# Kernel tuning notes

Hardware: AMD Instinct MI355X
Metric: run time of the kernel (lower is better)

## Reference

```python
import jax, jax.numpy as jnp
import numpy as np

D_IN = 768
D_OUT = 768
N_HEADS = 12
HEAD_DIM = D_OUT // N_HEADS


def setup_inputs() -> dict:
    key = jax.random.key(0)
    ks = jax.random.split(key, 6)
    B, S = 2, 4096
    x = jax.random.normal(ks[0], (B, S, D_IN), dtype=jnp.float32)
    s = 0.02
    Wq = jax.random.normal(ks[1], (D_IN, D_OUT), dtype=jnp.float32) * s
    Wk = jax.random.normal(ks[2], (D_IN, D_OUT), dtype=jnp.float32) * s
    Wv = jax.random.normal(ks[3], (D_IN, D_OUT), dtype=jnp.float32) * s
    Wo = jax.random.normal(ks[4], (D_OUT, D_OUT), dtype=jnp.float32) * s
    bo = jnp.zeros((D_OUT,), dtype=jnp.float32)
    return {"x": x, "Wq": Wq, "Wk": Wk, "Wv": Wv, "Wo": Wo, "bo": bo}


def reference(x, Wq, Wk, Wv, Wo, bo):
    B, S, _ = x.shape
    # QKV projections (no bias), reshape to [B, H, S, Dh]
    q = (x @ Wq).reshape(B, S, N_HEADS, HEAD_DIM).transpose(0, 2, 1, 3)
    k = (x @ Wk).reshape(B, S, N_HEADS, HEAD_DIM).transpose(0, 2, 1, 3)
    v = (x @ Wv).reshape(B, S, N_HEADS, HEAD_DIM).transpose(0, 2, 1, 3)
    # scores: [B, H, S, S], causal mask, scaled softmax
    scores = jnp.einsum('bhqd,bhkd->bhqk', q, k)
    causal = jnp.triu(jnp.ones((S, S), dtype=bool), k=1)
    scores = jnp.where(causal, -jnp.inf, scores)
    attn = jax.nn.softmax(scores / np.sqrt(HEAD_DIM).astype(np.float32), axis=-1)
    # dropout p=0.0 -> identity
    ctx = jnp.einsum('bhqk,bhkd->bqhd', attn, v).reshape(B, S, D_OUT)
    return ctx @ Wo + bo
```

## Files before the change

kernel.cpp:

```cpp
#include <hip/hip_runtime.h>

#define S 4096
#define BATCH 2
#define D 768
#define NH 12
#define DH 64
#define NROWS (BATCH * S)
#define N_ITEMS (32 * NH * BATCH)
#define CTR_OFF 67633152

typedef __attribute__((ext_vector_type(8))) short bf16x8;
typedef __attribute__((ext_vector_type(4))) float f32x4;
typedef __attribute__((ext_vector_type(2))) unsigned uint32x2;

__device__ __forceinline__ unsigned short f2bf(float f) {
    unsigned u = __builtin_bit_cast(unsigned, f);
    u += 0x7fff + ((u >> 16) & 1);
    return (unsigned short)(u >> 16);
}

__device__ __forceinline__ float fexp2(float x) {
#if __has_builtin(__builtin_amdgcn_exp2f)
    return __builtin_amdgcn_exp2f(x);
#else
    return exp2f(x);
#endif
}

#define GLDS16(g, l)                                                   \
    __builtin_amdgcn_global_load_lds(                                  \
        (const __attribute__((address_space(1))) void*)(g),            \
        (__attribute__((address_space(3))) void*)(l), 16, 0, 0)

__global__ __launch_bounds__(256) void cvt_x(const float* __restrict__ x,
                                             unsigned short* __restrict__ xb)
{
    int i = (blockIdx.x * 256 + threadIdx.x) * 4;
    float4 v = *(const float4*)(x + i);
    ushort4 o = make_ushort4(f2bf(v.x), f2bf(v.y), f2bf(v.z), f2bf(v.w));
    *(ushort4*)(xb + i) = o;
}

__global__ __launch_bounds__(256) void cvt_w(
    const float* __restrict__ Wq, const float* __restrict__ Wk,
    const float* __restrict__ Wv, const float* __restrict__ Wo,
    unsigned short* __restrict__ wt)
{
    __shared__ float tile[32][33];
    const int z = blockIdx.z;
    const float* W = (z == 0) ? Wq : (z == 1) ? Wk : (z == 2) ? Wv : Wo;
    const int k0 = blockIdx.x * 32, n0 = blockIdx.y * 32;
    const int t = threadIdx.x;
    const int r = t >> 3, c4 = (t & 7) * 4;

    float4 v = *(const float4*)(W + (size_t)(k0 + r) * D + n0 + c4);
    tile[r][c4 + 0] = v.x; tile[r][c4 + 1] = v.y;
    tile[r][c4 + 2] = v.z; tile[r][c4 + 3] = v.w;
    __syncthreads();
    ushort4 o = make_ushort4(f2bf(tile[c4 + 0][r]), f2bf(tile[c4 + 1][r]),
                             f2bf(tile[c4 + 2][r]), f2bf(tile[c4 + 3][r]));
    *(ushort4*)(wt + ((size_t)z * D + n0 + r) * D + k0 + c4) = o;
}

__global__ __launch_bounds__(256) void gemm_qkv(
    const unsigned short* __restrict__ xb,
    const unsigned short* __restrict__ wt,
    unsigned short* __restrict__ qb, unsigned short* __restrict__ kb,
    unsigned short* __restrict__ vtb)
{
    __shared__ unsigned short As[128 * 64];
    __shared__ unsigned short Bs[128 * 64];

    const int t = threadIdx.x;
    const int lane = t & 63, w = t >> 6;
    const int l16 = lane & 15, quad = lane >> 4;
    const int wm = w & 1, wn = w >> 1;
    const int m0 = blockIdx.x * 128;
    const int n0g = blockIdx.y * 128;
    const int z = n0g / 768;
    const int c0 = n0g - z * 768;
    const unsigned short* Wz = wt + (size_t)z * D * D;

    f32x4 acc[4][4] = {};

    for (int k0 = 0; k0 < D; k0 += 64) {
#pragma unroll
        for (int i = 0; i < 4; ++i) {
            int g = i * 256 + w * 64 + lane;
            int row = g >> 3, cl = g & 7, cg = cl ^ (row & 7);
            GLDS16(xb + (size_t)(m0 + row) * D + k0 + cg * 8,
                   As + (size_t)(i * 256 + w * 64) * 8);
            GLDS16(Wz + (size_t)(c0 + row) * D + k0 + cg * 8,
                   Bs + (size_t)(i * 256 + w * 64) * 8);
        }
        __syncthreads();
#pragma unroll
        for (int kk = 0; kk < 2; ++kk) {
            bf16x8 af[4], bf_[4];
#pragma unroll
            for (int mt = 0; mt < 4; ++mt) {
                int r = wm * 64 + mt * 16 + l16;
                int c = kk * 4 + quad;
                af[mt] = *(const bf16x8*)&As[(r * 8 + (c ^ (r & 7))) * 8];
            }
#pragma unroll
            for (int nt = 0; nt < 4; ++nt) {
                int r = wn * 64 + nt * 16 + l16;
                int c = kk * 4 + quad;
                bf_[nt] = *(const bf16x8*)&Bs[(r * 8 + (c ^ (r & 7))) * 8];
            }
#pragma unroll
            for (int mt = 0; mt < 4; ++mt)
#pragma unroll
                for (int nt = 0; nt < 4; ++nt)
                    acc[mt][nt] = __builtin_amdgcn_mfma_f32_16x16x32_bf16(
                        af[mt], bf_[nt], acc[mt][nt], 0, 0, 0);
        }
        __syncthreads();
    }

    if (z < 2) {
        unsigned short* outp = (z == 0) ? qb : kb;
        const float scale = (z == 0) ? 0.18033688011112042f : 1.0f;
#pragma unroll
        for (int mt = 0; mt < 4; ++mt) {
#pragma unroll
            for (int reg = 0; reg < 4; ++reg) {
                int m = wm * 64 + mt * 16 + quad * 4 + reg;
                int ng = m0 + m;
                int b = ng >> 12, s = ng & 4095;
#pragma unroll
                for (int nt = 0; nt < 4; ++nt) {
                    int n = c0 + wn * 64 + nt * 16 + l16;
                    int h = n >> 6, dh = n & 63;
                    outp[(((size_t)b * NH + h) * S + s) * DH + dh] =
                        f2bf(acc[mt][nt][reg] * scale);
                }
            }
        }
    } else {
#pragma unroll
        for (int mt = 0; mt < 4; ++mt) {
#pragma unroll
            for (int nt = 0; nt < 4; ++nt) {
                int m = wm * 64 + mt * 16 + quad * 4;
                int ng = m0 + m;
                int b = ng >> 12, s = ng & 4095;
                int n = c0 + wn * 64 + nt * 16 + l16;
                int h = n >> 6, dh = n & 63;
                ushort4 p = make_ushort4(
                    f2bf(acc[mt][nt][0]), f2bf(acc[mt][nt][1]),
                    f2bf(acc[mt][nt][2]), f2bf(acc[mt][nt][3]));
                *(ushort4*)(vtb + (((size_t)b * NH + h) * DH + dh) * S + s) = p;
            }
        }
    }
}

__global__ __launch_bounds__(512, 4) void attn_mfma(
    const unsigned short* __restrict__ qg,
    const unsigned short* __restrict__ kg,
    const unsigned short* __restrict__ vtg,
    unsigned short* __restrict__ ctxb,
    int* __restrict__ work_ctr)
{
    __shared__ unsigned short Ks[2][64 * 64];
    __shared__ unsigned short Vs[2][64 * 64];
    __shared__ int s_item;

    const float INF = __builtin_inff();
    const int t = threadIdx.x;
    const int w = t >> 6, lane = t & 63;
    const int l16 = lane & 15, quad = lane >> 4;
    const int a7 = l16 & 7;
    const int srow = t >> 3;
    const int scg = (t & 7) ^ (srow & 7);

    bf16x8 vone;
#pragma unroll
    for (int i = 0; i < 8; ++i) vone[i] = (short)0x3F80;

    for (;;) {
        if (t == 0) s_item = atomicAdd(work_ctr, 1);
        __syncthreads();
        const int p = s_item;
        if (p >= N_ITEMS) return;

        const int qt = 31 - (p / (NH * BATCH));
        const int hb = p % (NH * BATCH);
        const int h = hb % NH, b = hb / NH;
        const size_t hbase = ((size_t)b * NH + h) * (size_t)S * DH;
        const unsigned short* kp = kg + hbase;
        const unsigned short* vp = vtg + hbase;

        const int qrow = qt * 128 + w * 16 + l16;
        bf16x8 bq[2];
#pragma unroll
        for (int kk = 0; kk < 2; ++kk)
            bq[kk] = *(const bf16x8*)(qg + hbase + (size_t)qrow * DH +
                                      kk * 32 + quad * 8);

        f32x4 acc_o[4] = {};
        f32x4 acc_sum = {};

        const int jmax = 2 * qt + 1, jd = 2 * qt;

        GLDS16(kp + (size_t)srow * DH + scg * 8, &Ks[0][(size_t)w * 64 * 8]);
        GLDS16(vp + (size_t)srow * S + scg * 8, &Vs[0][(size_t)w * 64 * 8]);

        for (int j = 0; j <= jmax; ++j) {
            const int cur = j & 1;
            __syncthreads();
            if (j < jmax) {
                GLDS16(kp + (size_t)((j + 1) * 64 + srow) * DH + scg * 8,
                       &Ks[cur ^ 1][(size_t)w * 64 * 8]);
                GLDS16(vp + (size_t)srow * S + (j + 1) * 64 + scg * 8,
                       &Vs[cur ^ 1][(size_t)w * 64 * 8]);
            }

            const unsigned short* Kc = Ks[cur];
            const unsigned short* Vc = Vs[cur];

            f32x4 acc_s[4] = {};
            __builtin_amdgcn_s_setprio(1);
#pragma unroll
            for (int kk = 0; kk < 2; ++kk)
#pragma unroll
                for (int ms = 0; ms < 4; ++ms) {
                    int r = ms * 16 + l16, c = kk * 4 + quad;
                    bf16x8 ak = *(const bf16x8*)&Kc[(r * 8 + (c ^ a7)) * 8];
                    acc_s[ms] = __builtin_amdgcn_mfma_f32_16x16x32_bf16(
                        ak, bq[kk], acc_s[ms], 0, 0, 0);
                }
            __builtin_amdgcn_s_setprio(0);

            if (j >= jd) {
#pragma unroll
                for (int ms = 0; ms < 4; ++ms)
#pragma unroll
                    for (int reg = 0; reg < 4; ++reg)
                        if ((j * 64 + ms * 16 + quad * 4 + reg) > qrow)
                            acc_s[ms][reg] = -INF;
            }

            bf16x8 bp[2];
            {
                unsigned ulo[4], uhi[4];
#pragma unroll
                for (int ms = 0; ms < 4; ++ms) {
                    float e0 = fexp2(acc_s[ms][0]);
                    float e1 = fexp2(acc_s[ms][1]);
                    float e2 = fexp2(acc_s[ms][2]);
                    float e3 = fexp2(acc_s[ms][3]);
                    asm("v_cvt_pk_bf16_f32 %0, %1, %2"
                        : "=v"(ulo[ms]) : "v"(e0), "v"(e1));
                    asm("v_cvt_pk_bf16_f32 %0, %1, %2"
                        : "=v"(uhi[ms]) : "v"(e2), "v"(e3));
                }
#pragma unroll
                for (int kp2 = 0; kp2 < 2; ++kp2) {
                    uint32x2 lo = __builtin_amdgcn_permlane32_swap(
                        ulo[2 * kp2], ulo[2 * kp2 + 1], false, false);
                    uint32x2 s02 = __builtin_amdgcn_permlane16_swap(
                        lo[0], lo[1], false, false);
                    uint32x2 hi = __builtin_amdgcn_permlane32_swap(
                        uhi[2 * kp2], uhi[2 * kp2 + 1], false, false);
                    uint32x2 s13 = __builtin_amdgcn_permlane16_swap(
                        hi[0], hi[1], false, false);
                    union { unsigned u[4]; bf16x8 v; } pb;
                    pb.u[0] = s02[0]; pb.u[1] = s13[0];
                    pb.u[2] = s02[1]; pb.u[3] = s13[1];
                    bp[kp2] = pb.v;
                }
            }

            __builtin_amdgcn_s_setprio(1);
#pragma unroll
            for (int kk = 0; kk < 2; ++kk) {
#pragma unroll
                for (int d = 0; d < 4; ++d) {
                    int r = d * 16 + l16, c = kk * 4 + quad;
                    bf16x8 av = *(const bf16x8*)&Vc[(r * 8 + (c ^ a7)) * 8];
                    acc_o[d] = __builtin_amdgcn_mfma_f32_16x16x32_bf16(
                        av, bp[kk], acc_o[d], 0, 0, 0);
                }
                acc_sum = __builtin_amdgcn_mfma_f32_16x16x32_bf16(
                    vone, bp[kk], acc_sum, 0, 0, 0);
            }
            __builtin_amdgcn_s_setprio(0);
        }

        {
            float inv = 1.f / acc_sum[0];
            size_t base = ((size_t)(b * S + qrow)) * D + h * 64;
#pragma unroll
            for (int d = 0; d < 4; ++d) {
                ushort4 o;
                o.x = f2bf(acc_o[d][0] * inv);
                o.y = f2bf(acc_o[d][1] * inv);
                o.z = f2bf(acc_o[d][2] * inv);
                o.w = f2bf(acc_o[d][3] * inv);
                *(ushort4*)(ctxb + base + d * 16 + quad * 4) = o;
            }
        }
    }
}

__global__ __launch_bounds__(256) void gemm_out(
    const unsigned short* __restrict__ ctxb,
    const unsigned short* __restrict__ wt,
    const float* __restrict__ bo,
    float* __restrict__ out)
{
    __shared__ unsigned short As[128 * 64];
    __shared__ unsigned short Bs[64 * 64];

    const int t = threadIdx.x;
    const int lane = t & 63, w = t >> 6;
    const int l16 = lane & 15, quad = lane >> 4;
    const int m0 = blockIdx.x * 128;
    const int n0 = blockIdx.y * 64;
    const unsigned short* Wz = wt + (size_t)3 * D * D;

    f32x4 acc[2][4] = {};

    for (int k0 = 0; k0 < D; k0 += 64) {
#pragma unroll
        for (int i = 0; i < 4; ++i) {
            int g = i * 256 + w * 64 + lane;
            int row = g >> 3, cl = g & 7, cg = cl ^ (row & 7);
            GLDS16(ctxb + (size_t)(m0 + row) * D + k0 + cg * 8,
                   As + (size_t)(i * 256 + w * 64) * 8);
            if (i < 2)
                GLDS16(Wz + (size_t)(n0 + row) * D + k0 + cg * 8,
                       Bs + (size_t)(i * 256 + w * 64) * 8);
        }
        __syncthreads();
#pragma unroll
        for (int kk = 0; kk < 2; ++kk) {
            bf16x8 af[2], bf_[4];
#pragma unroll
            for (int mt = 0; mt < 2; ++mt) {
                int r = w * 32 + mt * 16 + l16;
                int c = kk * 4 + quad;
                af[mt] = *(const bf16x8*)&As[(r * 8 + (c ^ (r & 7))) * 8];
            }
#pragma unroll
            for (int nt = 0; nt < 4; ++nt) {
                int r = nt * 16 + l16;
                int c = kk * 4 + quad;
                bf_[nt] = *(const bf16x8*)&Bs[(r * 8 + (c ^ (r & 7))) * 8];
            }
#pragma unroll
            for (int mt = 0; mt < 2; ++mt)
#pragma unroll
                for (int nt = 0; nt < 4; ++nt)
                    acc[mt][nt] = __builtin_amdgcn_mfma_f32_16x16x32_bf16(
                        af[mt], bf_[nt], acc[mt][nt], 0, 0, 0);
        }
        __syncthreads();
    }

    float bv[4];
#pragma unroll
    for (int nt = 0; nt < 4; ++nt)
        bv[nt] = bo[n0 + nt * 16 + l16];
#pragma unroll
    for (int mt = 0; mt < 2; ++mt)
#pragma unroll
        for (int reg = 0; reg < 4; ++reg) {
            int m = m0 + w * 32 + mt * 16 + quad * 4 + reg;
#pragma unroll
            for (int nt = 0; nt < 4; ++nt)
                out[(size_t)m * D + n0 + nt * 16 + l16] =
                    acc[mt][nt][reg] + bv[nt];
        }
}

extern "C" void kernel_launch(void* const* d_in, const int* in_sizes, int n_in,
                              void* d_out, int out_size, void* d_ws, size_t ws_size,
                              hipStream_t stream)
{
    const float* x  = (const float*)d_in[0];
    const float* Wq = (const float*)d_in[1];
    const float* Wk = (const float*)d_in[2];
    const float* Wv = (const float*)d_in[3];
    const float* Wo = (const float*)d_in[4];
    const float* bo = (const float*)d_in[5];
    float* out = (float*)d_out;

    const size_t elems = (size_t)NROWS * D;
    unsigned short* xb   = (unsigned short*)d_ws;
    unsigned short* wt   = xb + elems;
    unsigned short* q    = wt + (size_t)4 * D * D;
    unsigned short* k    = q + elems;
    unsigned short* vt   = k + elems;
    unsigned short* ctxb = vt + elems;
    int* work_ctr = (int*)((char*)d_ws + CTR_OFF);

    hipMemsetAsync(work_ctr, 0, sizeof(int), stream);

    cvt_x<<<NROWS * D / 1024, 256, 0, stream>>>(x, xb);
    dim3 gw(D / 32, D / 32, 4);
    cvt_w<<<gw, 256, 0, stream>>>(Wq, Wk, Wv, Wo, wt);

    dim3 g1(NROWS / 128, (3 * D) / 128);
    gemm_qkv<<<g1, 256, 0, stream>>>(xb, wt, q, k, vt);

    attn_mfma<<<512, 512, 0, stream>>>(q, k, vt, ctxb, work_ctr);

    dim3 g3(NROWS / 128, D / 64);
    gemm_out<<<g3, 256, 0, stream>>>(ctxb, wt, bo, out);
}
```

Baseline: 232.9 us.

## Split KV range for longest causal query tiles and merge halves in combine kernel

The dynamic work queue now has 960 items instead of 768. The eight longest query tiles per head and batch are split into two halves of the KV range, and the remaining tiles are scheduled in decreasing length order. Each split half writes unnormalized fp32 output and row sums into scratch space reused from the x and weight conversion buffers. A new combine kernel adds the two halves and normalizes them into ctxb. The aim is to shorten the tail caused by long causal tiles. The cost is an extra kernel launch and roughly 12 MB of extra fp32 partial traffic.

```diff
diff --git a/kernel.cpp b/kernel.cpp
--- a/kernel.cpp
+++ b/kernel.cpp
@@ -6,8 +6,10 @@
 #define NH 12
 #define DH 64
 #define NROWS (BATCH * S)
-#define N_ITEMS (32 * NH * BATCH)
 #define CTR_OFF 67633152
+
+#define N_ITEMS 960
+#define NSPLIT 192
 
 typedef __attribute__((ext_vector_type(8))) short bf16x8;
 typedef __attribute__((ext_vector_type(4))) float f32x4;
@@ -162,6 +164,8 @@
     const unsigned short* __restrict__ kg,
     const unsigned short* __restrict__ vtg,
     unsigned short* __restrict__ ctxb,
+    float* __restrict__ Opart,
+    float* __restrict__ Spart,
     int* __restrict__ work_ctr)
 {
     __shared__ unsigned short Ks[2][64 * 64];
@@ -186,9 +190,19 @@
         const int p = s_item;
         if (p >= N_ITEMS) return;
 
-        const int qt = 31 - (p / (NH * BATCH));
-        const int hb = p % (NH * BATCH);
+        int qt, hb, jlo, jhi, half = 0;
+        bool partial;
+        if (p < 216)      { qt = 23 - p / 24; hb = p % 24;
+                            jlo = 0; jhi = 2 * qt + 1; partial = false; }
+        else if (p < 600) { int q = p - 216; qt = 31 - q / 48;
+                            int r = q % 48; half = r / 24; hb = r % 24;
+                            partial = true;
+                            jlo = half ? qt + 1 : 0;
+                            jhi = half ? 2 * qt + 1 : qt; }
+        else              { int q = p - 600; qt = 14 - q / 24; hb = q % 24;
+                            jlo = 0; jhi = 2 * qt + 1; partial = false; }
         const int h = hb % NH, b = hb / NH;
+        const int jd = 2 * qt;
         const size_t hbase = ((size_t)b * NH + h) * (size_t)S * DH;
         const unsigned short* kp = kg + hbase;
         const unsigned short* vp = vtg + hbase;
@@ -203,15 +217,15 @@
         f32x4 acc_o[4] = {};
         f32x4 acc_sum = {};
 
-        const int jmax = 2 * qt + 1, jd = 2 * qt;
-
-        GLDS16(kp + (size_t)srow * DH + scg * 8, &Ks[0][(size_t)w * 64 * 8]);
-        GLDS16(vp + (size_t)srow * S + scg * 8, &Vs[0][(size_t)w * 64 * 8]);
-
-        for (int j = 0; j <= jmax; ++j) {
+        GLDS16(kp + (size_t)(jlo * 64 + srow) * DH + scg * 8,
+               &Ks[jlo & 1][(size_t)w * 64 * 8]);
+        GLDS16(vp + (size_t)srow * S + jlo * 64 + scg * 8,
+               &Vs[jlo & 1][(size_t)w * 64 * 8]);
+
+        for (int j = jlo; j <= jhi; ++j) {
             const int cur = j & 1;
             __syncthreads();
-            if (j < jmax) {
+            if (j < jhi) {
                 GLDS16(kp + (size_t)((j + 1) * 64 + srow) * DH + scg * 8,
                        &Ks[cur ^ 1][(size_t)w * 64 * 8]);
                 GLDS16(vp + (size_t)srow * S + (j + 1) * 64 + scg * 8,
@@ -290,7 +304,7 @@
             __builtin_amdgcn_s_setprio(0);
         }
 
-        {
+        if (!partial) {
             float inv = 1.f / acc_sum[0];
             size_t base = ((size_t)(b * S + qrow)) * D + h * 64;
 #pragma unroll
@@ -302,7 +316,42 @@
                 o.w = f2bf(acc_o[d][3] * inv);
                 *(ushort4*)(ctxb + base + d * 16 + quad * 4) = o;
             }
-        }
+        } else {
+            int sid = (31 - qt) * 24 + hb;
+            int qr = w * 16 + l16;
+            float* Op = Opart + ((size_t)(half * NSPLIT + sid)) * (128 * 64)
+                              + (size_t)qr * 64;
+#pragma unroll
+            for (int d = 0; d < 4; ++d)
+#pragma unroll
+                for (int reg = 0; reg < 4; ++reg)
+                    Op[d * 16 + quad * 4 + reg] = acc_o[d][reg];
+            if (quad == 0)
+                Spart[(size_t)(half * NSPLIT + sid) * 128 + qr] = acc_sum[0];
+        }
+    }
+}
+
+__global__ __launch_bounds__(256) void attn_combine(
+    const float* __restrict__ Opart, const float* __restrict__ Spart,
+    unsigned short* __restrict__ ctxb)
+{
+    const int sid = blockIdx.x;
+    const int qt = 31 - sid / 24, hb = sid % 24;
+    const int h = hb % NH, b = hb / NH;
+    const int t = threadIdx.x;
+    const float* O0 = Opart + (size_t)sid * 8192;
+    const float* O1 = Opart + (size_t)(NSPLIT + sid) * 8192;
+    const float* S0 = Spart + (size_t)sid * 128;
+    const float* S1 = Spart + (size_t)(NSPLIT + sid) * 128;
+
+#pragma unroll
+    for (int i = 0; i < 32; ++i) {
+        int e = i * 256 + t;
+        int qr = e >> 6, dh = e & 63;
+        float inv = 1.f / (S0[qr] + S1[qr]);
+        float v = (O0[e] + O1[e]) * inv;
+        ctxb[((size_t)(b * S + qt * 128 + qr)) * D + h * 64 + dh] = f2bf(v);
     }
 }
 
@@ -397,6 +446,8 @@
     unsigned short* vt   = k + elems;
     unsigned short* ctxb = vt + elems;
     int* work_ctr = (int*)((char*)d_ws + CTR_OFF);
+    float* Opart = (float*)xb;
+    float* Spart = (float*)wt;
 
     hipMemsetAsync(work_ctr, 0, sizeof(int), stream);
 
@@ -407,7 +458,8 @@
     dim3 g1(NROWS / 128, (3 * D) / 128);
     gemm_qkv<<<g1, 256, 0, stream>>>(xb, wt, q, k, vt);
 
-    attn_mfma<<<512, 512, 0, stream>>>(q, k, vt, ctxb, work_ctr);
+    attn_mfma<<<512, 512, 0, stream>>>(q, k, vt, ctxb, Opart, Spart, work_ctr);
+    attn_combine<<<NSPLIT, 256, 0, stream>>>(Opart, Spart, ctxb);
 
     dim3 g3(NROWS / 128, D / 64);
     gemm_out<<<g3, 256, 0, stream>>>(ctxb, wt, bo, out);
```

After: 239.9 us. 3.0% more time.
